# Performance work log

Hardware: AMD Instinct MI355X
Metric: run time of the kernel (lower is better)

Reference implementation:

```python
import jax, jax.numpy as jnp
import numpy as np

N_EMBD = 2048
N_HEAD = 16
N_KV_HEAD = 4
HEAD_DIM = N_EMBD // N_HEAD
MAX_SEQ_LEN = 2048
EPS = 1e-6
ROPE_THETA = 10000.0


def _build_rope_cache(dim, max_seq_len, theta=ROPE_THETA):
    inv_freq = 1.0 / theta ** (np.arange(0, dim, 2, dtype=np.float32) / dim)
    t = np.arange(max_seq_len, dtype=np.float32)
    freqs = np.outer(t, inv_freq)
    emb = np.concatenate([freqs, freqs], axis=-1)
    return jnp.asarray(np.cos(emb)), jnp.asarray(np.sin(emb))


def _rotate_half(x):
    x1, x2 = jnp.split(x, 2, axis=-1)
    return jnp.concatenate([-x2, x1], axis=-1)


def _rms_norm(x, w, eps=EPS):
    var = jnp.mean(jnp.square(x), axis=-1, keepdims=True)
    return x * jax.lax.rsqrt(var + eps) * w


def setup_inputs() -> dict:
    key = jax.random.key(0)
    ks = jax.random.split(key, 7)
    s = 1.0 / np.sqrt(N_EMBD)
    kv_dim = N_KV_HEAD * HEAD_DIM
    x = jax.random.normal(ks[0], (2, 2048, N_EMBD), dtype=jnp.float32)
    Wq = jax.random.normal(ks[1], (N_EMBD, N_EMBD), dtype=jnp.float32) * s
    Wk = jax.random.normal(ks[2], (kv_dim, N_EMBD), dtype=jnp.float32) * s
    Wv = jax.random.normal(ks[3], (kv_dim, N_EMBD), dtype=jnp.float32) * s
    Wo = jax.random.normal(ks[4], (N_EMBD, N_EMBD), dtype=jnp.float32) * s
    qn_w = jnp.ones((HEAD_DIM,), dtype=jnp.float32)
    kn_w = jnp.ones((HEAD_DIM,), dtype=jnp.float32)
    cos, sin = _build_rope_cache(HEAD_DIM, MAX_SEQ_LEN)
    return {"x": x, "Wq": Wq, "Wk": Wk, "Wv": Wv, "Wo": Wo,
            "qn_w": qn_w, "kn_w": kn_w, "rope_cos": cos, "rope_sin": sin}


def reference(x, Wq, Wk, Wv, Wo, qn_w, kn_w, rope_cos, rope_sin):
    B, T, C = x.shape
    # projections (torch Linear: y = x @ W.T)
    q = jnp.einsum('btc,dc->btd', x, Wq).reshape(B, T, N_HEAD, HEAD_DIM).transpose(0, 2, 1, 3)
    k = jnp.einsum('btc,dc->btd', x, Wk).reshape(B, T, N_KV_HEAD, HEAD_DIM).transpose(0, 2, 1, 3)
    v = jnp.einsum('btc,dc->btd', x, Wv).reshape(B, T, N_KV_HEAD, HEAD_DIM).transpose(0, 2, 1, 3)
    # qk rms-norm
    q = _rms_norm(q, qn_w)
    k = _rms_norm(k, kn_w)
    # rope
    cos = rope_cos[:T][None, None]  # [1,1,T,D]
    sin = rope_sin[:T][None, None]
    q = q * cos + _rotate_half(q) * sin
    k = k * cos + _rotate_half(k) * sin
    # GQA broadcast: group queries over kv heads instead of repeating k/v
    G = N_HEAD // N_KV_HEAD
    qg = q.reshape(B, N_KV_HEAD, G, T, HEAD_DIM)
    scale = 1.0 / jnp.sqrt(jnp.asarray(HEAD_DIM, dtype=q.dtype))
    scores = jnp.einsum('bhgqd,bhkd->bhgqk', qg, k) * scale  # [B,KV,G,T,T]
    causal = jnp.tril(jnp.ones((T, T), dtype=bool))
    scores = jnp.where(causal, scores, jnp.asarray(-jnp.inf, dtype=scores.dtype))
    attn = jax.nn.softmax(scores, axis=-1)
    y = jnp.einsum('bhgqk,bhkd->bhgqd', attn, v)  # [B,KV,G,T,D]
    y = y.reshape(B, N_HEAD, T, HEAD_DIM).transpose(0, 2, 1, 3).reshape(B, T, C)
    return jnp.einsum('btc,dc->btd', y, Wo)
```

## Files before the change

### kernel.cpp

```cpp
#include <hip/hip_runtime.h>
#include <stdint.h>

typedef unsigned short u16;
typedef __attribute__((ext_vector_type(4))) float f32x4;
typedef __attribute__((ext_vector_type(16))) float f32x16;
typedef __attribute__((ext_vector_type(8))) short bf16x8;
typedef __attribute__((ext_vector_type(4))) unsigned short u16x4;
typedef __attribute__((ext_vector_type(4))) unsigned u32x4;

static __device__ __forceinline__ u16 f2bf(float f) {
  union { float f; unsigned u; } v; v.f = f;
  unsigned r = v.u + 0x7fffu + ((v.u >> 16) & 1u);
  return (u16)(r >> 16);
}

static __device__ __forceinline__ unsigned cvtpk(float lo, float hi) {
  unsigned r;
  asm("v_cvt_pk_bf16_f32 %0, %1, %2" : "=v"(r) : "v"(lo), "v"(hi));
  return r;
}

static __device__ __forceinline__ void plane32_swap(unsigned& a, unsigned& b) {
  asm volatile("v_permlane32_swap_b32 %0, %1" : "+v"(a), "+v"(b));
}

static __device__ __forceinline__ void load_lds16(const void* g, void* l) {
  __builtin_amdgcn_global_load_lds(
      (const __attribute__((address_space(1))) void*)g,
      (__attribute__((address_space(3))) void*)l, 16, 0, 0);
}


__global__ __launch_bounds__(256) void cvt_f32_bf16(
    const float* __restrict__ in, u16* __restrict__ out, int n) {
  int i = blockIdx.x * 256 + threadIdx.x;
  const int n4 = n >> 2;
  for (; i < n4; i += gridDim.x * 256) {
    f32x4 v = *(const f32x4*)(in + (size_t)i * 4);
    u16x4 o = { f2bf(v[0]), f2bf(v[1]), f2bf(v[2]), f2bf(v[3]) };
    *(u16x4*)(out + (size_t)i * 4) = o;
  }
}

__global__ __launch_bounds__(256) void build_wcat(
    const float* __restrict__ Wq, const float* __restrict__ Wk,
    const float* __restrict__ Wv, u16* __restrict__ out) {
  int i = blockIdx.x * 256 + threadIdx.x;
  const int n4 = 3072 * 512;
  for (; i < n4; i += gridDim.x * 256) {
    int row = i >> 9;
    int c4 = i & 511;
    const float* src;
    if (row < 2048)       src = Wq + (size_t)row * 2048;
    else if (row < 2560)  src = Wk + (size_t)(row - 2048) * 2048;
    else                  src = Wv + (size_t)(row - 2560) * 2048;
    f32x4 v = *(const f32x4*)(src + c4 * 4);
    u16x4 o = { f2bf(v[0]), f2bf(v[1]), f2bf(v[2]), f2bf(v[3]) };
    *(u16x4*)(out + (size_t)i * 4) = o;
  }
}

__global__ __launch_bounds__(256) void gemm_bt(
    const u16* __restrict__ A, const u16* __restrict__ B,
    float* __restrict__ C, int M, int N, int K) {
  __shared__ u16 As[128 * 32];
  __shared__ u16 Bs[128 * 32];
  const int tid = threadIdx.x;
  const int lin = blockIdx.x;
  const int x = lin & 7, t = lin >> 3;
  const int bm = x * 4 + (t & 3);
  const int bn = t >> 2;
  const int w = tid >> 6, l = tid & 63;
  const int wr = w >> 1, wc = w & 1;
  const int lr = l & 15, lg = l >> 4;
  f32x4 acc[4][4] = {};
  const int srow = tid >> 2;
  const int scol = (tid & 3) << 3;
  const u16* Ag = A + (size_t)bm * 128 * K + (size_t)srow * K + scol;
  const u16* Bg = B + (size_t)bn * 128 * K + (size_t)srow * K + scol;
  u16* Asl = As + srow * 32 + scol;
  u16* Bsl = Bs + srow * 32 + scol;
  const int nk = K >> 5;
  for (int kt = 0; kt < nk; ++kt) {
    __syncthreads();
    const int ko = kt << 5;
    load_lds16(Ag + ko, Asl);
    load_lds16(Ag + (size_t)64 * K + ko, Asl + 64 * 32);
    load_lds16(Bg + ko, Bsl);
    load_lds16(Bg + (size_t)64 * K + ko, Bsl + 64 * 32);
    __syncthreads();
    bf16x8 af[4], bfr[4];
#pragma unroll
    for (int m = 0; m < 4; ++m)
      af[m] = *(const bf16x8*)&As[(wr * 64 + m * 16 + lr) * 32 + lg * 8];
#pragma unroll
    for (int n = 0; n < 4; ++n)
      bfr[n] = *(const bf16x8*)&Bs[(wc * 64 + n * 16 + lr) * 32 + lg * 8];
#pragma unroll
    for (int m = 0; m < 4; ++m)
#pragma unroll
      for (int n = 0; n < 4; ++n)
        acc[m][n] = __builtin_amdgcn_mfma_f32_16x16x32_bf16(af[m], bfr[n], acc[m][n], 0, 0, 0);
  }
#pragma unroll
  for (int m = 0; m < 4; ++m) {
    const int row = bm * 128 + wr * 64 + m * 16 + lg * 4;
#pragma unroll
    for (int n = 0; n < 4; ++n) {
      const int col = bn * 128 + wc * 64 + n * 16 + lr;
#pragma unroll
      for (int r = 0; r < 4; ++r)
        C[(size_t)(row + r) * N + col] = acc[m][n][r];
    }
  }
}

__global__ __launch_bounds__(256) void norm_rope(
    const float* __restrict__ qkv, const float* __restrict__ qn_w,
    const float* __restrict__ kn_w, const float* __restrict__ cosb,
    const float* __restrict__ sinb, u16* __restrict__ qhat,
    u16* __restrict__ khat) {
  const int gw = (blockIdx.x * 256 + threadIdx.x) >> 6;
  const int lane = threadIdx.x & 63;
  const int slot = gw % 20;
  const int row = gw / 20;
  const int t = row & 2047;
  const int b = row >> 11;
  const float* src; const float* nw; u16* dst;
  bool isq = slot < 16;
  if (isq) {
    src = qkv + (size_t)row * 3072 + slot * 128;
    nw = qn_w;
    dst = qhat + ((size_t)(b * 16 + slot) * 2048 + t) * 128;
  } else {
    src = qkv + (size_t)row * 3072 + 2048 + (slot - 16) * 128;
    nw = kn_w;
    dst = khat + ((size_t)(b * 4 + (slot - 16)) * 2048 + t) * 128;
  }
  float x1 = src[lane], x2 = src[lane + 64];
  float ss = x1 * x1 + x2 * x2;
#pragma unroll
  for (int o = 32; o; o >>= 1) ss += __shfl_xor(ss, o);
  float rs = rsqrtf(ss * (1.0f / 128.0f) + 1e-6f);
  float h1 = x1 * rs * nw[lane];
  float h2 = x2 * rs * nw[lane + 64];
  float c = cosb[t * 128 + lane], s = sinb[t * 128 + lane];
  float o1 = h1 * c - h2 * s;
  float o2 = h2 * c + h1 * s;
  if (isq) { o1 *= 0.088388347648318447f; o2 *= 0.088388347648318447f; }
  dst[lane] = f2bf(o1);
  dst[lane + 64] = f2bf(o2);
}

__global__ __launch_bounds__(256) void v_trans(
    const float* __restrict__ qkv, u16* __restrict__ vT) {
  __shared__ u16 st[64][130];
  const int bi = blockIdx.x;
  const int tt = bi & 31;
  const int kv = (bi >> 5) & 3;
  const int b = bi >> 7;
  const int tid = threadIdx.x;
#pragma unroll
  for (int i = 0; i < 32; ++i) {
    int idx = i * 256 + tid;
    int t = idx >> 7, d = idx & 127;
    float v = qkv[(size_t)(b * 2048 + tt * 64 + t) * 3072 + 2560 + kv * 128 + d];
    st[t][d] = f2bf(v);
  }
  __syncthreads();
#pragma unroll
  for (int i = 0; i < 32; ++i) {
    int idx = i * 256 + tid;
    int d = idx >> 6, t = idx & 63;
    vT[((size_t)(b * 4 + kv) * 128 + d) * 2048 + tt * 64 + t] = st[t][d];
  }
}

__global__ __launch_bounds__(512, 2) void attn(
    const u16* __restrict__ qhat, const u16* __restrict__ khat,
    const u16* __restrict__ vT, u16* __restrict__ yb) {
  __shared__ u16 Kt[2][64 * 128];
  const int bi = blockIdx.x;
  const int s = bi & 7;
  const int bh = bi >> 3;
  const int h = bh & 15, b = bh >> 4;
  const int kvh = h >> 2;
  const int tid = threadIdx.x;
  const int w = tid >> 6, l = tid & 63;
  const int ws = w & 3;
  const int cw = (w < 4) ? s : (15 - s);
  const int ql = l & 31, hi = l >> 5;
  const int wq0 = cw * 128 + ws * 32;
  const int wq_end = wq0 + 31;
  const int qg = wq0 + ql;

  bf16x8 qf[8];
  const u16* qp = qhat + ((size_t)(b * 16 + h) * 2048 + qg) * 128 + hi * 8;
#pragma unroll
  for (int sf = 0; sf < 8; ++sf) qf[sf] = *(const bf16x8*)(qp + 16 * sf);

  f32x16 yacc[4] = {};
  float m = -1e30f, lsum = 0.f;

  const u16* Kg = khat + (size_t)(b * 4 + kvh) * 2048 * 128;
  const u16* Vg = vT + (size_t)(b * 4 + kvh) * 128 * 2048;
  const int nt = 32 - 2 * s;

  auto stageK = [&](int tile, int buf) {
#pragma unroll
    for (int j = 0; j < 2; ++j) {
      int idx = j * 512 + tid;
      int row = idx >> 4, ch = idx & 15;
      load_lds16(Kg + (size_t)(tile * 64 + row) * 128 + ((ch ^ (row & 7)) * 8),
                 &Kt[buf][idx * 8]);
    }
  };

  stageK(0, 0);
  int cur = 0;
  for (int tile = 0; tile < nt; ++tile) {
    const int kv0 = tile * 64;
    __syncthreads();
    if (tile + 1 < nt) stageK(tile + 1, cur ^ 1);
    if (kv0 <= wq_end) {
      const u16* Vrow = Vg + (size_t)ql * 2048 + kv0 + hi * 8;
      bf16x8 va[4], vb[4];
#pragma unroll
      for (int ks = 0; ks < 4; ++ks) va[ks] = *(const bf16x8*)(Vrow + ks * 16);
#pragma unroll
      for (int ks = 0; ks < 4; ++ks) vb[ks] = *(const bf16x8*)(Vrow + 32 * 2048 + ks * 16);
      const u16* Kc = Kt[cur];
      f32x16 sacc[2] = {};
      __builtin_amdgcn_s_setprio(1);
#pragma unroll
      for (int n = 0; n < 2; ++n) {
#pragma unroll
        for (int sf = 0; sf < 8; ++sf) {
          bf16x8 kf = *(const bf16x8*)&Kc[(n * 32 + ql) * 128 + (((2 * sf + hi) ^ (l & 7)) * 8)];
          sacc[n] = __builtin_amdgcn_mfma_f32_32x32x16_bf16(kf, qf[sf], sacc[n], 0, 0, 0);
        }
      }
      __builtin_amdgcn_s_setprio(0);
      if (kv0 + 63 > wq0) {
#pragma unroll
        for (int n = 0; n < 2; ++n)
#pragma unroll
          for (int r = 0; r < 16; ++r) {
            int kv = kv0 + n * 32 + (r & 3) + 8 * (r >> 2) + 4 * hi;
            if (kv > qg) sacc[n][r] = -1e30f;
          }
      }
      float pm = -1e30f;
#pragma unroll
      for (int n = 0; n < 2; ++n)
#pragma unroll
        for (int r = 0; r < 16; ++r) pm = fmaxf(pm, sacc[n][r]);
      pm = fmaxf(pm, __shfl_xor(pm, 32));
      if (!__all(pm - m <= 8.0f)) {
        float mn = fmaxf(m, pm);
        float sc = __expf(m - mn);
        m = mn;
        lsum *= sc;
#pragma unroll
        for (int r = 0; r < 16; ++r) {
          int row = (r & 3) + 8 * (r >> 2) + 4 * hi;
          float scr = __shfl(sc, row);
#pragma unroll
          for (int d = 0; d < 4; ++d) yacc[d][r] *= scr;
        }
      }
      float ls = 0.f;
#pragma unroll
      for (int n = 0; n < 2; ++n)
#pragma unroll
        for (int r = 0; r < 16; ++r) {
          float e = __expf(sacc[n][r] - m);
          sacc[n][r] = e;
          ls += e;
        }
      ls += __shfl_xor(ls, 32);
      lsum += ls;
      bf16x8 pa[4];
#pragma unroll
      for (int s4 = 0; s4 < 4; ++s4) {
        const int n = s4 >> 1, R = (s4 & 1) * 8;
        unsigned P01 = cvtpk(sacc[n][R + 0], sacc[n][R + 1]);
        unsigned P23 = cvtpk(sacc[n][R + 2], sacc[n][R + 3]);
        unsigned P45 = cvtpk(sacc[n][R + 4], sacc[n][R + 5]);
        unsigned P67 = cvtpk(sacc[n][R + 6], sacc[n][R + 7]);
        plane32_swap(P01, P45);
        plane32_swap(P23, P67);
        union { u32x4 u; bf16x8 bv; } cvu;
        cvu.u[0] = P01; cvu.u[1] = P23; cvu.u[2] = P45; cvu.u[3] = P67;
        pa[s4] = cvu.bv;
      }
      __builtin_amdgcn_s_setprio(1);
#pragma unroll
      for (int ks = 0; ks < 4; ++ks)
        yacc[0] = __builtin_amdgcn_mfma_f32_32x32x16_bf16(pa[ks], va[ks], yacc[0], 0, 0, 0);
#pragma unroll
      for (int ks = 0; ks < 4; ++ks) va[ks] = *(const bf16x8*)(Vrow + 64 * 2048 + ks * 16);
#pragma unroll
      for (int ks = 0; ks < 4; ++ks)
        yacc[1] = __builtin_amdgcn_mfma_f32_32x32x16_bf16(pa[ks], vb[ks], yacc[1], 0, 0, 0);
#pragma unroll
      for (int ks = 0; ks < 4; ++ks) vb[ks] = *(const bf16x8*)(Vrow + 96 * 2048 + ks * 16);
#pragma unroll
      for (int ks = 0; ks < 4; ++ks)
        yacc[2] = __builtin_amdgcn_mfma_f32_32x32x16_bf16(pa[ks], va[ks], yacc[2], 0, 0, 0);
#pragma unroll
      for (int ks = 0; ks < 4; ++ks)
        yacc[3] = __builtin_amdgcn_mfma_f32_32x32x16_bf16(pa[ks], vb[ks], yacc[3], 0, 0, 0);
      __builtin_amdgcn_s_setprio(0);
    }
    cur ^= 1;
  }
#pragma unroll
  for (int r = 0; r < 16; ++r) {
    int row = (r & 3) + 8 * (r >> 2) + 4 * hi;
    float li = __shfl(lsum, row);
    float inv = 1.0f / li;
    u16* yp = yb + ((size_t)(b * 2048) + wq0 + row) * 2048 + h * 128 + ql;
#pragma unroll
    for (int d = 0; d < 4; ++d) yp[d * 32] = f2bf(yacc[d][r] * inv);
  }
}


extern "C" void kernel_launch(void* const* d_in, const int* in_sizes, int n_in,
                              void* d_out, int out_size, void* d_ws, size_t ws_size,
                              hipStream_t stream) {
  const float* x    = (const float*)d_in[0];
  const float* Wq   = (const float*)d_in[1];
  const float* Wk   = (const float*)d_in[2];
  const float* Wv   = (const float*)d_in[3];
  const float* Wo   = (const float*)d_in[4];
  const float* qn   = (const float*)d_in[5];
  const float* kn   = (const float*)d_in[6];
  const float* cosb = (const float*)d_in[7];
  const float* sinb = (const float*)d_in[8];
  float* out = (float*)d_out;
  (void)in_sizes; (void)n_in; (void)out_size; (void)ws_size;

  char* p = (char*)d_ws;
  u16*   xb   = (u16*)p;   p += (size_t)8388608 * 2;
  u16*   wcat = (u16*)p;   p += (size_t)6291456 * 2;
  u16*   wob  = (u16*)p;   p += (size_t)4194304 * 2;
  float* qkvf = (float*)p; p += (size_t)12582912 * 4;
  u16*   qh   = (u16*)p;   p += (size_t)8388608 * 2;
  u16*   kh   = (u16*)p;   p += (size_t)2097152 * 2;
  u16*   vt   = (u16*)p;   p += (size_t)2097152 * 2;
  u16*   yb   = (u16*)p;   p += (size_t)8388608 * 2;

  cvt_f32_bf16<<<2048, 256, 0, stream>>>(x, xb, 8388608);
  build_wcat<<<2048, 256, 0, stream>>>(Wq, Wk, Wv, wcat);
  cvt_f32_bf16<<<2048, 256, 0, stream>>>(Wo, wob, 4194304);
  gemm_bt<<<768, 256, 0, stream>>>(xb, wcat, qkvf, 4096, 3072, 2048);
  norm_rope<<<20480, 256, 0, stream>>>(qkvf, qn, kn, cosb, sinb, qh, kh);
  v_trans<<<256, 256, 0, stream>>>(qkvf, vt);
  attn<<<256, 512, 0, stream>>>(qh, kh, vt, yb);
  gemm_bt<<<512, 256, 0, stream>>>(yb, wob, out, 4096, 2048, 2048);
}
```

Measured before the change: 261.1 us.

## Add 256x256 pipelined GEMM for QKV, use exp2 softmax, prefetch all V fragments

Adds a new 256x256-tile GEMM kernel with 512 threads, a 4-slot LDS ring and fine-grained barrier and waitcnt interleaving of loads and MFMAs, and uses it for the QKV projection instead of the 128x128 kernel. Separately, folds log2(e) into the query scale so the attention softmax can use the raw v_exp_f32 (exp2) instruction, and raises the lazy-rescale threshold to match the base-2 domain. It also loads all four V fragment sets before the QK MFMAs and interleaves the PV MFMAs, at the cost of more registers in attention.

```diff
diff --git a/kernel.cpp b/kernel.cpp
--- a/kernel.cpp
+++ b/kernel.cpp
@@ -22,6 +22,12 @@
 
 static __device__ __forceinline__ void plane32_swap(unsigned& a, unsigned& b) {
   asm volatile("v_permlane32_swap_b32 %0, %1" : "+v"(a), "+v"(b));
+}
+
+static __device__ __forceinline__ float exp2_fast(float x) {
+  float r;
+  asm("v_exp_f32 %0, %1" : "=v"(r) : "v"(x));
+  return r;
 }
 
 static __device__ __forceinline__ void load_lds16(const void* g, void* l) {
@@ -58,6 +64,99 @@
     u16x4 o = { f2bf(v[0]), f2bf(v[1]), f2bf(v[2]), f2bf(v[3]) };
     *(u16x4*)(out + (size_t)i * 4) = o;
   }
+}
+
+__global__ __launch_bounds__(512, 2) void gemm256(
+    const u16* __restrict__ A, const u16* __restrict__ B,
+    float* __restrict__ C, int M, int N, int K) {
+  __shared__ u16 S[65536];
+  const int nbn = N >> 8;
+  const int chunk = ((M >> 8) * nbn) >> 3;
+  const int bid = blockIdx.x;
+  const int wg = (bid & 7) * chunk + (bid >> 3);
+  const int bm = wg / nbn, bn = wg % nbn;
+  const int tid = threadIdx.x;
+  const int w = tid >> 6, l = tid & 63;
+  const int wm = w >> 2, wn = w & 3;
+  const int lr = l & 15, lg = l >> 4;
+
+  f32x4 acc[8][4] = {};
+  bf16x8 af[8], bfr[2];
+
+  auto stage = [&](int tile, int isB, int kh) {
+    tile &= 31;
+    const u16* G = isB ? B : A;
+    const int rbase = (isB ? bn : bm) << 8;
+    const int col0 = tile * 64 + kh * 32;
+    u16* slot = S + (isB ? 32768 : 0) + ((((tile & 1) << 1) + kh) << 13);
+#pragma unroll
+    for (int j = 0; j < 2; ++j) {
+      const int o = (j << 12) + tid * 8;
+      const int cq = o >> 11, row = (o >> 3) & 255;
+      load_lds16(G + (size_t)(rbase + row) * K + col0 + cq * 8, slot + o);
+    }
+  };
+  auto lda = [&](int pi, int kh) {
+    const u16* Sa = S + (((pi << 1) + kh) << 13);
+#pragma unroll
+    for (int m = 0; m < 8; ++m)
+      af[m] = *(const bf16x8*)(Sa + ((lg * 256 + wm * 128 + m * 16 + lr) << 3));
+  };
+  auto ldb = [&](int pi, int kh, int nh) {
+    const u16* Sb = S + 32768 + (((pi << 1) + kh) << 13);
+#pragma unroll
+    for (int j = 0; j < 2; ++j)
+      bfr[j] = *(const bf16x8*)(Sb + ((lg * 256 + wn * 64 + (nh * 2 + j) * 16 + lr) << 3));
+  };
+  auto mm = [&](int nh) {
+    asm volatile("s_waitcnt lgkmcnt(0)" ::: "memory");
+    __builtin_amdgcn_sched_barrier(0);
+    __builtin_amdgcn_s_setprio(1);
+#pragma unroll
+    for (int m = 0; m < 8; ++m) {
+      acc[m][nh * 2 + 0] = __builtin_amdgcn_mfma_f32_16x16x32_bf16(af[m], bfr[0], acc[m][nh * 2 + 0], 0, 0, 0);
+      acc[m][nh * 2 + 1] = __builtin_amdgcn_mfma_f32_16x16x32_bf16(af[m], bfr[1], acc[m][nh * 2 + 1], 0, 0, 0);
+    }
+    __builtin_amdgcn_s_setprio(0);
+    __builtin_amdgcn_s_barrier();
+  };
+
+  stage(0, 0, 0); stage(0, 1, 0); stage(0, 0, 1); stage(0, 1, 1);
+  stage(1, 0, 0); stage(1, 1, 0);
+  asm volatile("s_waitcnt vmcnt(4)" ::: "memory");
+  __builtin_amdgcn_s_barrier();
+
+  for (int T0 = 0; T0 < 32; T0 += 2) {
+    const int p0 = 0;
+    lda(p0, 0); ldb(p0, 0, 0); stage(T0 + 1, 0, 1);
+    __builtin_amdgcn_s_barrier(); mm(0);
+    ldb(p0, 0, 1); stage(T0 + 1, 1, 1);
+    __builtin_amdgcn_s_barrier(); mm(1);
+    lda(p0, 1); ldb(p0, 1, 0); stage(T0 + 2, 0, 0);
+    __builtin_amdgcn_s_barrier(); mm(0);
+    ldb(p0, 1, 1); stage(T0 + 2, 1, 0);
+    asm volatile("s_waitcnt vmcnt(6)" ::: "memory");
+    __builtin_amdgcn_s_barrier(); mm(1);
+    lda(1, 0); ldb(1, 0, 0); stage(T0 + 2, 0, 1);
+    __builtin_amdgcn_s_barrier(); mm(0);
+    ldb(1, 0, 1); stage(T0 + 2, 1, 1);
+    __builtin_amdgcn_s_barrier(); mm(1);
+    lda(1, 1); ldb(1, 1, 0); stage(T0 + 3, 0, 0);
+    __builtin_amdgcn_s_barrier(); mm(0);
+    ldb(1, 1, 1); stage(T0 + 3, 1, 0);
+    asm volatile("s_waitcnt vmcnt(6)" ::: "memory");
+    __builtin_amdgcn_s_barrier(); mm(1);
+  }
+
+  const int rb = (bm << 8) + wm * 128 + lg * 4;
+  const int cb = (bn << 8) + wn * 64 + lr;
+#pragma unroll
+  for (int m = 0; m < 8; ++m)
+#pragma unroll
+    for (int nf = 0; nf < 4; ++nf)
+#pragma unroll
+      for (int r = 0; r < 4; ++r)
+        C[(size_t)(rb + m * 16 + r) * N + cb + nf * 16] = acc[m][nf][r];
 }
 
 __global__ __launch_bounds__(256) void gemm_bt(
@@ -147,7 +246,7 @@
   float c = cosb[t * 128 + lane], s = sinb[t * 128 + lane];
   float o1 = h1 * c - h2 * s;
   float o2 = h2 * c + h1 * s;
-  if (isq) { o1 *= 0.088388347648318447f; o2 *= 0.088388347648318447f; }
+  if (isq) { o1 *= 0.12751744752f; o2 *= 0.12751744752f; }
   dst[lane] = f2bf(o1);
   dst[lane + 64] = f2bf(o2);
 }
@@ -224,11 +323,15 @@
     if (tile + 1 < nt) stageK(tile + 1, cur ^ 1);
     if (kv0 <= wq_end) {
       const u16* Vrow = Vg + (size_t)ql * 2048 + kv0 + hi * 8;
-      bf16x8 va[4], vb[4];
-#pragma unroll
-      for (int ks = 0; ks < 4; ++ks) va[ks] = *(const bf16x8*)(Vrow + ks * 16);
-#pragma unroll
-      for (int ks = 0; ks < 4; ++ks) vb[ks] = *(const bf16x8*)(Vrow + 32 * 2048 + ks * 16);
+      bf16x8 vfr0[4], vfr1[4], vfr2[4], vfr3[4];
+#pragma unroll
+      for (int ks = 0; ks < 4; ++ks) vfr0[ks] = *(const bf16x8*)(Vrow + ks * 16);
+#pragma unroll
+      for (int ks = 0; ks < 4; ++ks) vfr1[ks] = *(const bf16x8*)(Vrow + 32 * 2048 + ks * 16);
+#pragma unroll
+      for (int ks = 0; ks < 4; ++ks) vfr2[ks] = *(const bf16x8*)(Vrow + 64 * 2048 + ks * 16);
+#pragma unroll
+      for (int ks = 0; ks < 4; ++ks) vfr3[ks] = *(const bf16x8*)(Vrow + 96 * 2048 + ks * 16);
       const u16* Kc = Kt[cur];
       f32x16 sacc[2] = {};
       __builtin_amdgcn_s_setprio(1);
@@ -256,9 +359,9 @@
 #pragma unroll
         for (int r = 0; r < 16; ++r) pm = fmaxf(pm, sacc[n][r]);
       pm = fmaxf(pm, __shfl_xor(pm, 32));
-      if (!__all(pm - m <= 8.0f)) {
+      if (!__all(pm - m <= 11.0f)) {
         float mn = fmaxf(m, pm);
-        float sc = __expf(m - mn);
+        float sc = exp2_fast(m - mn);
         m = mn;
         lsum *= sc;
 #pragma unroll
@@ -274,7 +377,7 @@
       for (int n = 0; n < 2; ++n)
 #pragma unroll
         for (int r = 0; r < 16; ++r) {
-          float e = __expf(sacc[n][r] - m);
+          float e = exp2_fast(sacc[n][r] - m);
           sacc[n][r] = e;
           ls += e;
         }
@@ -296,21 +399,12 @@
       }
       __builtin_amdgcn_s_setprio(1);
 #pragma unroll
-      for (int ks = 0; ks < 4; ++ks)
-        yacc[0] = __builtin_amdgcn_mfma_f32_32x32x16_bf16(pa[ks], va[ks], yacc[0], 0, 0, 0);
-#pragma unroll
-      for (int ks = 0; ks < 4; ++ks) va[ks] = *(const bf16x8*)(Vrow + 64 * 2048 + ks * 16);
-#pragma unroll
-      for (int ks = 0; ks < 4; ++ks)
-        yacc[1] = __builtin_amdgcn_mfma_f32_32x32x16_bf16(pa[ks], vb[ks], yacc[1], 0, 0, 0);
-#pragma unroll
-      for (int ks = 0; ks < 4; ++ks) vb[ks] = *(const bf16x8*)(Vrow + 96 * 2048 + ks * 16);
-#pragma unroll
-      for (int ks = 0; ks < 4; ++ks)
-        yacc[2] = __builtin_amdgcn_mfma_f32_32x32x16_bf16(pa[ks], va[ks], yacc[2], 0, 0, 0);
-#pragma unroll
-      for (int ks = 0; ks < 4; ++ks)
-        yacc[3] = __builtin_amdgcn_mfma_f32_32x32x16_bf16(pa[ks], vb[ks], yacc[3], 0, 0, 0);
+      for (int ks = 0; ks < 4; ++ks) {
+        yacc[0] = __builtin_amdgcn_mfma_f32_32x32x16_bf16(pa[ks], vfr0[ks], yacc[0], 0, 0, 0);
+        yacc[1] = __builtin_amdgcn_mfma_f32_32x32x16_bf16(pa[ks], vfr1[ks], yacc[1], 0, 0, 0);
+        yacc[2] = __builtin_amdgcn_mfma_f32_32x32x16_bf16(pa[ks], vfr2[ks], yacc[2], 0, 0, 0);
+        yacc[3] = __builtin_amdgcn_mfma_f32_32x32x16_bf16(pa[ks], vfr3[ks], yacc[3], 0, 0, 0);
+      }
       __builtin_amdgcn_s_setprio(0);
     }
     cur ^= 1;
@@ -355,7 +449,7 @@
   cvt_f32_bf16<<<2048, 256, 0, stream>>>(x, xb, 8388608);
   build_wcat<<<2048, 256, 0, stream>>>(Wq, Wk, Wv, wcat);
   cvt_f32_bf16<<<2048, 256, 0, stream>>>(Wo, wob, 4194304);
-  gemm_bt<<<768, 256, 0, stream>>>(xb, wcat, qkvf, 4096, 3072, 2048);
+  gemm256<<<192, 512, 0, stream>>>(xb, wcat, qkvf, 4096, 3072, 2048);
   norm_rope<<<20480, 256, 0, stream>>>(qkvf, qn, kn, cosb, sinb, qh, kh);
   v_trans<<<256, 256, 0, stream>>>(qkvf, vt);
   attn<<<256, 512, 0, stream>>>(qh, kh, vt, yb);
```

Result: slower. 277.3 us (+6.2%).
